# Performance work log

Hardware: AMD Instinct MI355X
Metric: run time of the kernel (lower is better)

## Reference

```python
import jax, jax.numpy as jnp
import numpy as np
from jax import lax

B_, H_, W_, C_ = 2, 64, 64, 96
DI, N_, R_, K_ = 192, 16, 6, 4  # d_inner=expand*C, d_state, dt_rank=ceil(96/16), 4 scan dirs


def _ln(x, g, b, eps):
    m = jnp.mean(x, axis=-1, keepdims=True)
    v = jnp.var(x, axis=-1, keepdims=True)
    return (x - m) / jnp.sqrt(v + eps) * g + b


def _conv1x1(x, w, b=None):
    y = jnp.einsum('bihw,oi->bohw', x, w)
    return y if b is None else y + b[None, :, None, None]


def _dwconv(x, w):
    return lax.conv_general_dilated(x, w, (1, 1), 'SAME',
                                    feature_group_count=x.shape[1],
                                    dimension_numbers=('NCHW', 'OIHW', 'NCHW'))


def _ss2d(x, in_proj_w, conv2d_w, conv2d_b, x_proj_w, dt_proj_w, dt_proj_b,
          A_logs, Ds, out_norm_g, out_norm_b, out_proj_w):
    B, H, W, C = x.shape
    L = H * W
    xz = jnp.einsum('bhwc,dc->bhwd', x, in_proj_w)          # [B,H,W,2*DI]
    xx, z = jnp.split(xz, 2, axis=-1)
    xc = jnp.transpose(xx, (0, 3, 1, 2))                    # [B,DI,H,W]
    xc = jax.nn.silu(_dwconv(xc, conv2d_w) + conv2d_b[None, :, None, None])
    # 4 scan directions: row-major, col-major, and their reverses
    x_hwwh = jnp.stack([xc.reshape(B, DI, L),
                        jnp.transpose(xc, (0, 1, 3, 2)).reshape(B, DI, L)], axis=1)
    xs = jnp.concatenate([x_hwwh, jnp.flip(x_hwwh, axis=-1)], axis=1)  # [B,K,DI,L]
    x_dbl = jnp.einsum('bkdl,kcd->bkcl', xs, x_proj_w)
    dts, Bs, Cs = jnp.split(x_dbl, [R_, R_ + N_], axis=2)   # [B,K,R,L],[B,K,N,L],[B,K,N,L]
    dt = jnp.einsum('bkrl,kdr->bkdl', dts, dt_proj_w) + dt_proj_b[None, :, :, None]
    dt = jax.nn.softplus(dt)
    A = -jnp.exp(A_logs).reshape(K_, DI, N_)

    def step(h, inp):
        u_t, dt_t, B_t, C_t = inp                            # [B,K,DI],[B,K,DI],[B,K,N],[B,K,N]
        dA = jnp.exp(dt_t[..., None] * A)                    # [B,K,DI,N]
        h = h * dA + (dt_t * u_t)[..., None] * B_t[:, :, None, :]
        y = jnp.einsum('bkdn,bkn->bkd', h, C_t)
        return h, y

    inps = (jnp.moveaxis(xs, -1, 0), jnp.moveaxis(dt, -1, 0),
            jnp.moveaxis(Bs, -1, 0), jnp.moveaxis(Cs, -1, 0))
    h0 = jnp.zeros((B, K_, DI, N_), xs.dtype)
    _, ys = lax.scan(step, h0, inps)                         # [L,B,K,DI]
    out_y = jnp.moveaxis(ys, 0, -1) + xs * Ds.reshape(K_, DI)[None, :, :, None]
    inv = jnp.flip(out_y[:, 2:4], axis=-1)
    y1 = out_y[:, 0]
    y2 = inv[:, 0]
    y3 = jnp.transpose(out_y[:, 1].reshape(B, DI, W, H), (0, 1, 3, 2)).reshape(B, DI, L)
    y4 = jnp.transpose(inv[:, 1].reshape(B, DI, W, H), (0, 1, 3, 2)).reshape(B, DI, L)
    y = jnp.transpose(y1 + y2 + y3 + y4, (0, 2, 1)).reshape(B, H, W, DI)
    y = _ln(y, out_norm_g, out_norm_b, 1e-5)
    y = y * jax.nn.silu(z)
    return jnp.einsum('bhwd,cd->bhwc', y, out_proj_w)


def _fftm(x, f1_w, f1_b, fm_w, fm_b, f2_w, f2_b):
    x = jax.nn.silu(_conv1x1(x, f1_w, f1_b))                 # [B,C/2,H,W]
    f = jnp.fft.rfftn(x, axes=(-2, -1), norm='ortho')        # [B,C/2,H,W//2+1] complex
    B, Ch, Hh, Wf = f.shape
    fr = jnp.stack([f.real, f.imag], axis=2).reshape(B, 2 * Ch, Hh, Wf)
    fr = jax.nn.silu(_conv1x1(fr, fm_w, fm_b))
    fr = fr.reshape(B, Ch, 2, Hh, Wf)
    fc = lax.complex(fr[:, :, 0], fr[:, :, 1])
    out = jnp.fft.irfftn(fc, s=x.shape[-2:], axes=(-2, -1), norm='ortho')
    return _conv1x1(out, f2_w, f2_b)


def _mgcb(x, in_w, dw3_w, dw5_w, out_w, ca_w1, ca_b1, ca_w2, ca_b2):
    Hd = 2 * x.shape[1]                                      # hidden_features = 2*dim
    p = _conv1x1(x, in_w)                                    # [B,2*Hd,H,W]
    s1 = 3 * Hd // 2
    x1, x2 = p[:, :s1], p[:, s1:]
    d1 = _dwconv(x1, dw3_w)
    x1_1, x1_2 = d1[:, :Hd], d1[:, Hd:]
    x2 = _dwconv(x2, dw5_w)
    y = jax.nn.gelu(x1_1, approximate=False) * jnp.concatenate([x1_2, x2], axis=1)
    y = _conv1x1(y, out_w)
    a = jnp.mean(y, axis=(2, 3))                             # channel attention (squeeze 30)
    a = jax.nn.relu(a @ ca_w1.T + ca_b1)
    a = jax.nn.sigmoid(a @ ca_w2.T + ca_b2)
    return y * a[:, :, None, None]


def _forward(input, ln1_g, ln1_b, skip_scale, skip_scale2, ln2_g, ln2_b,
             in_proj_w, conv2d_w, conv2d_b, x_proj_w, dt_proj_w, dt_proj_b,
             A_logs, Ds, out_norm_g, out_norm_b, out_proj_w,
             f1_w, f1_b, fm_w, fm_b, f2_w, f2_b,
             mg_in_w, mg_dw3_w, mg_dw5_w, mg_out_w,
             ca_w1, ca_b1, ca_w2, ca_b2, h_size, w_size):
    B, L, C = input.shape
    x4 = input.reshape(B, h_size, w_size, C)
    xn = _ln(x4, ln1_g, ln1_b, 1e-6)
    attn = _ss2d(xn, in_proj_w, conv2d_w, conv2d_b, x_proj_w, dt_proj_w,
                 dt_proj_b, A_logs, Ds, out_norm_g, out_norm_b, out_proj_w)
    fft = _fftm(jnp.transpose(xn, (0, 3, 1, 2)), f1_w, f1_b, fm_w, fm_b, f2_w, f2_b)
    x = x4 * skip_scale + attn + jnp.transpose(fft, (0, 2, 3, 1))
    xn2 = _ln(x, ln2_g, ln2_b, 1e-5)
    conv = _mgcb(jnp.transpose(xn2, (0, 3, 1, 2)), mg_in_w, mg_dw3_w, mg_dw5_w,
                 mg_out_w, ca_w1, ca_b1, ca_w2, ca_b2)
    x = x * skip_scale2 + jnp.transpose(conv, (0, 2, 3, 1))
    return x.reshape(B, L, C)


def setup_inputs() -> dict:
    key = jax.random.key(0)
    ks = iter(jax.random.split(key, 48))
    def rn(shape, s=0.02):
        return jax.random.normal(next(ks), shape, jnp.float32) * s
    d = {}
    d['input'] = jax.random.normal(next(ks), (B_, H_ * W_, C_), jnp.float32)
    d['ln1_g'] = jnp.ones((C_,)); d['ln1_b'] = jnp.zeros((C_,))
    d['skip_scale'] = jnp.ones((C_,)); d['skip_scale2'] = jnp.ones((C_,))
    d['ln2_g'] = jnp.ones((C_,)); d['ln2_b'] = jnp.zeros((C_,))
    d['in_proj_w'] = rn((2 * DI, C_))
    d['conv2d_w'] = rn((DI, 1, 3, 3), 0.1); d['conv2d_b'] = jnp.zeros((DI,))
    d['x_proj_w'] = rn((K_, R_ + 2 * N_, DI))
    d['dt_proj_w'] = rn((K_, DI, R_), 0.1)
    d['dt_proj_b'] = jnp.full((K_, DI), -4.6, jnp.float32) + rn((K_, DI), 0.5)
    d['A_logs'] = jnp.log(jnp.tile(jnp.arange(1, N_ + 1, dtype=jnp.float32), (K_ * DI, 1)))
    d['Ds'] = jnp.ones((K_ * DI,))
    d['out_norm_g'] = jnp.ones((DI,)); d['out_norm_b'] = jnp.zeros((DI,))
    d['out_proj_w'] = rn((C_, DI))
    Ch = C_ // 2
    d['f1_w'] = rn((Ch, C_)); d['f1_b'] = jnp.zeros((Ch,))
    d['fm_w'] = rn((C_, C_)); d['fm_b'] = jnp.zeros((C_,))
    d['f2_w'] = rn((C_, Ch)); d['f2_b'] = jnp.zeros((C_,))
    Hd = 2 * C_
    d['mg_in_w'] = rn((2 * Hd, C_))
    d['mg_dw3_w'] = rn((3 * Hd // 2, 1, 3, 3), 0.1)
    d['mg_dw5_w'] = rn((Hd // 2, 1, 5, 5), 0.1)
    d['mg_out_w'] = rn((C_, Hd))
    Csq = C_ // 30
    d['ca_w1'] = rn((Csq, C_)); d['ca_b1'] = jnp.zeros((Csq,))
    d['ca_w2'] = rn((C_, Csq)); d['ca_b2'] = jnp.zeros((C_,))
    d['h_size'] = H_
    d['w_size'] = W_
    return d


def reference(input, ln1_g, ln1_b, skip_scale, skip_scale2, ln2_g, ln2_b,
              in_proj_w, conv2d_w, conv2d_b, x_proj_w, dt_proj_w, dt_proj_b,
              A_logs, Ds, out_norm_g, out_norm_b, out_proj_w,
              f1_w, f1_b, fm_w, fm_b, f2_w, f2_b,
              mg_in_w, mg_dw3_w, mg_dw5_w, mg_out_w,
              ca_w1, ca_b1, ca_w2, ca_b2, h_size, w_size):
    return _forward(input, ln1_g, ln1_b, skip_scale, skip_scale2, ln2_g, ln2_b,
                    in_proj_w, conv2d_w, conv2d_b, x_proj_w, dt_proj_w, dt_proj_b,
                    A_logs, Ds, out_norm_g, out_norm_b, out_proj_w,
                    f1_w, f1_b, fm_w, fm_b, f2_w, f2_b,
                    mg_in_w, mg_dw3_w, mg_dw5_w, mg_out_w,
                    ca_w1, ca_b1, ca_w2, ca_b2, h_size, w_size)
```

## Files before the change

kernel.cpp:

```cpp
#include <hip/hip_runtime.h>
#include <math.h>

#define DEV __device__ __forceinline__

constexpr int DI = 192, Nn = 16, Rr = 6;
constexpr int Cc = 96;
constexpr int Ll = 4096;
constexpr int NC = 64;

DEV float silu_(float x) { return x / (1.f + __expf(-x)); }
DEV float wsum64(float v) {
  #pragma unroll
  for (int m = 32; m; m >>= 1) v += __shfl_xor(v, m, 64);
  return v;
}
DEV float qadd1(float v) {
  int i = __builtin_amdgcn_mov_dpp(__float_as_int(v), 0xB1, 0xF, 0xF, true);
  return v + __int_as_float(i);
}
DEV float qadd2(float v) {
  int i = __builtin_amdgcn_mov_dpp(__float_as_int(v), 0x4E, 0xF, 0xF, true);
  return v + __int_as_float(i);
}

template<int CIN, int COUT, int CB, int PXB, int IN_MODE, int OUT_MODE, int ACT, int HAS_BIAS, int LN>
__global__ void conv1x1v2_kernel(const float* __restrict__ in, const float4* __restrict__ wt,
                                 const float* __restrict__ bias, float* __restrict__ out,
                                 float* __restrict__ out2, const float* __restrict__ lng,
                                 const float* __restrict__ lnb) {
  constexpr int J4 = CIN / 4, STR = J4 + 1, CCN = CB / 16, PXT = PXB / 16;
  constexpr int NPB = 8192 / PXB;
  __shared__ float4 xv[PXB * STR];
  int t = threadIdx.x;
  int pb = blockIdx.x % NPB;
  int cbase = (blockIdx.x / NPB) * CB;
  int pbase = pb * PXB;
  if (IN_MODE == 0) {
    for (int idx = t; idx < PXB * J4; idx += 256) {
      int px = idx / J4, j4 = idx - px * J4;
      xv[px * STR + j4] = ((const float4*)in)[(size_t)(pbase + px) * J4 + j4];
    }
  } else {
    for (int idx = t; idx < PXB * CIN; idx += 256) {
      int px = idx & (PXB - 1), c = idx / PXB;
      int gp = pbase + px; int b = gp >> 12, p = gp & 4095;
      ((float*)xv)[px * (STR * 4) + c] = in[((size_t)b * CIN + c) * Ll + p];
    }
  }
  __syncthreads();
  if constexpr (LN) {
    constexpr int TPX = 256 / PXB;
    constexpr int CHUNK = CIN / TPX;
    int px = t / TPX, sub = t % TPX;
    float* row = (float*)(xv + px * STR);
    float sm = 0.f, sq = 0.f;
    #pragma unroll
    for (int j2 = 0; j2 < CHUNK; ++j2) {
      float v = row[sub + j2 * TPX];
      sm += v; sq += v * v;
    }
    #pragma unroll
    for (int m = 1; m < TPX; m <<= 1) {
      sm += __shfl_xor(sm, m, 64);
      sq += __shfl_xor(sq, m, 64);
    }
    float mean = sm * (1.f / CIN);
    float rs = rsqrtf(sq * (1.f / CIN) - mean * mean + 1e-6f);
    #pragma unroll
    for (int j2 = 0; j2 < CHUNK; ++j2) {
      int j = sub + j2 * TPX;
      row[j] = (row[j] - mean) * rs * lng[j] + lnb[j];
    }
    __syncthreads();
  }
  int g = t >> 4, ci = t & 15;
  float acc[PXT][CCN];
  #pragma unroll
  for (int cc = 0; cc < CCN; ++cc) {
    float b0 = HAS_BIAS ? bias[cbase + ci + 16 * cc] : 0.f;
    #pragma unroll
    for (int p = 0; p < PXT; ++p) acc[p][cc] = b0;
  }
  #pragma unroll 2
  for (int j4 = 0; j4 < J4; ++j4) {
    float4 xr[PXT];
    #pragma unroll
    for (int p = 0; p < PXT; ++p) xr[p] = xv[(g + 16 * p) * STR + j4];
    #pragma unroll
    for (int cc = 0; cc < CCN; ++cc) {
      float4 w4 = wt[(size_t)j4 * COUT + cbase + ci + 16 * cc];
      #pragma unroll
      for (int p = 0; p < PXT; ++p)
        acc[p][cc] += xr[p].x * w4.x + xr[p].y * w4.y + xr[p].z * w4.z + xr[p].w * w4.w;
    }
  }
  #pragma unroll
  for (int p = 0; p < PXT; ++p) {
    int gp = pbase + g + 16 * p;
    #pragma unroll
    for (int cc = 0; cc < CCN; ++cc) {
      int c = cbase + ci + 16 * cc;
      float v = acc[p][cc];
      if (OUT_MODE == 2) {
        if (c < 192) out[(size_t)gp * 192 + c] = v;
        else out2[(size_t)gp * 192 + (c - 192)] = silu_(v);
      } else {
        if (ACT == 1) v = silu_(v);
        if (OUT_MODE == 0) out[(size_t)gp * COUT + c] = v;
        else { int bb = gp >> 12, p2 = gp & 4095; out[((size_t)bb * COUT + c) * Ll + p2] = v; }
      }
    }
  }
}

__global__ void outproj_fused_kernel(
    const float* __restrict__ outy, const float* __restrict__ zs,
    const float* __restrict__ ong, const float* __restrict__ onb,
    const float4* __restrict__ wt, const float* __restrict__ input,
    const float* __restrict__ fftout, const float* __restrict__ ss,
    const float* __restrict__ ln2g, const float* __restrict__ ln2b,
    float* __restrict__ xres, float* __restrict__ xn2) {
  __shared__ float4 xv[32 * 49];
  int t = threadIdx.x;
  int pbase = blockIdx.x * 32;
  {
    int px = t >> 3, sub = t & 7;
    int pix = pbase + px;
    int p = pix & 4095, b = pix >> 12;
    int pt = ((p & 63) << 6) | (p >> 6);
    size_t base = (size_t)b * 4 * Ll * DI;
    const float* y0 = outy + base + (size_t)p * DI;
    const float* y1 = outy + base + ((size_t)Ll + pt) * DI;
    const float* y2 = outy + base + ((size_t)2 * Ll + (4095 - p)) * DI;
    const float* y3 = outy + base + ((size_t)3 * Ll + (4095 - pt)) * DI;
    float v[24];
    float sm = 0.f, sq = 0.f;
    #pragma unroll
    for (int j = 0; j < 24; ++j) {
      int c = sub + 8 * j;
      float vv = y0[c] + y1[c] + y2[c] + y3[c];
      v[j] = vv; sm += vv; sq += vv * vv;
    }
    #pragma unroll
    for (int m = 1; m < 8; m <<= 1) {
      sm += __shfl_xor(sm, m, 64);
      sq += __shfl_xor(sq, m, 64);
    }
    float mean = sm * (1.f / 192.f);
    float rs = rsqrtf(sq * (1.f / 192.f) - mean * mean + 1e-5f);
    const float* zrow = zs + (size_t)pix * DI;
    float* row = (float*)(xv + px * 49);
    #pragma unroll
    for (int j = 0; j < 24; ++j) {
      int c = sub + 8 * j;
      row[c] = ((v[j] - mean) * rs * ong[c] + onb[c]) * zrow[c];
    }
  }
  __syncthreads();
  int g = t >> 4, ci = t & 15;
  float acc[2][6];
  #pragma unroll
  for (int pI = 0; pI < 2; ++pI)
    #pragma unroll
    for (int cc = 0; cc < 6; ++cc) acc[pI][cc] = 0.f;
  #pragma unroll 2
  for (int j4 = 0; j4 < 48; ++j4) {
    float4 xr0 = xv[g * 49 + j4];
    float4 xr1 = xv[(g + 16) * 49 + j4];
    #pragma unroll
    for (int cc = 0; cc < 6; ++cc) {
      float4 w4 = wt[(size_t)j4 * 96 + ci + 16 * cc];
      acc[0][cc] += xr0.x * w4.x + xr0.y * w4.y + xr0.z * w4.z + xr0.w * w4.w;
      acc[1][cc] += xr1.x * w4.x + xr1.y * w4.y + xr1.z * w4.z + xr1.w * w4.w;
    }
  }
  #pragma unroll
  for (int pI = 0; pI < 2; ++pI) {
    int gp = pbase + g + 16 * pI;
    float vv[6];
    float sm = 0.f, sq = 0.f;
    #pragma unroll
    for (int cc = 0; cc < 6; ++cc) {
      int c = ci + 16 * cc;
      float x = input[(size_t)gp * Cc + c] * ss[c] + acc[pI][cc] + fftout[(size_t)gp * Cc + c];
      vv[cc] = x; sm += x; sq += x * x;
    }
    #pragma unroll
    for (int m = 1; m < 16; m <<= 1) {
      sm += __shfl_xor(sm, m, 64);
      sq += __shfl_xor(sq, m, 64);
    }
    float mean = sm * (1.f / 96.f);
    float rs = rsqrtf(sq * (1.f / 96.f) - mean * mean + 1e-5f);
    #pragma unroll
    for (int cc = 0; cc < 6; ++cc) {
      int c = ci + 16 * cc;
      xres[(size_t)gp * Cc + c] = vv[cc];
      xn2[(size_t)gp * Cc + c] = (vv[cc] - mean) * rs * ln2g[c] + ln2b[c];
    }
  }
}

__global__ void wprep_all_kernel(const float* __restrict__ xpw, float4* __restrict__ xpwT,
                                 const float* __restrict__ cw, const float* __restrict__ mg3,
                                 const float* __restrict__ mg5, float* __restrict__ WC3T,
                                 float* __restrict__ W3T, float* __restrict__ W5T,
                                 const float* __restrict__ ipw, float4* __restrict__ WIPT,
                                 const float* __restrict__ mgiw, float4* __restrict__ WMGT,
                                 const float* __restrict__ opw, float4* __restrict__ WOPT,
                                 const float* __restrict__ mgow, float4* __restrict__ WMOT,
                                 const float* __restrict__ f1w, float4* __restrict__ WF1T,
                                 const float* __restrict__ f2w, float4* __restrict__ WF2T) {
  int idx = blockIdx.x * 256 + threadIdx.x;
  if (idx < 9216) {
    int k = idx / (48 * 48);
    int r = idx % (48 * 48);
    int j4 = r / 48, c = r % 48;
    float4 v = make_float4(0.f, 0.f, 0.f, 0.f);
    if (c < 38) v = ((const float4*)xpw)[((size_t)k * 38 + c) * 48 + j4];
    xpwT[((size_t)k * 48 + j4) * 48 + c] = v;
  }
  if (idx < 1728) { int c = idx / 9, j = idx % 9; WC3T[j * 192 + c] = cw[idx]; }
  if (idx < 2592) { int c = idx / 9, j = idx % 9; W3T[j * 288 + c] = mg3[idx]; }
  if (idx < 2400) { int c = idx / 25, j = idx % 25; W5T[j * 96 + c] = mg5[idx]; }
  if (idx < 9216) { int oc = idx % 384, j4 = idx / 384; WIPT[idx] = ((const float4*)ipw)[(size_t)oc * 24 + j4]; }
  if (idx < 9216) { int oc = idx % 384, j4 = idx / 384; WMGT[idx] = ((const float4*)mgiw)[(size_t)oc * 24 + j4]; }
  if (idx < 4608) { int oc = idx % 96, j4 = idx / 96; WOPT[idx] = ((const float4*)opw)[(size_t)oc * 48 + j4]; }
  if (idx < 4608) { int oc = idx % 96, j4 = idx / 96; WMOT[idx] = ((const float4*)mgow)[(size_t)oc * 48 + j4]; }
  if (idx < 1152) { int oc = idx % 48, j4 = idx / 48; WF1T[idx] = ((const float4*)f1w)[(size_t)oc * 24 + j4]; }
  if (idx < 1152) { int oc = idx % 96, j4 = idx / 96; WF2T[idx] = ((const float4*)f2w)[(size_t)oc * 12 + j4]; }
}

__global__ void dwconv3_silu_kernel(const float* __restrict__ xx, const float* __restrict__ wc3t,
                                    const float* __restrict__ bias, float* __restrict__ xc,
                                    float* __restrict__ xct) {
  int idx = blockIdx.x * 256 + threadIdx.x;
  int d4 = idx % 48;
  int p = (idx / 48) & (Ll - 1);
  int b = idx / (48 * Ll);
  int h = p >> 6, wq = p & 63;
  const float4* base = (const float4*)xx + (size_t)b * Ll * 48;
  const float4* wt = (const float4*)wc3t;
  float4 bv = ((const float4*)bias)[d4];
  float a0 = bv.x, a1 = bv.y, a2 = bv.z, a3 = bv.w;
  #pragma unroll
  for (int i = 0; i < 3; ++i) {
    int hh = h - 1 + i;
    if ((unsigned)hh >= 64u) continue;
    #pragma unroll
    for (int j = 0; j < 3; ++j) {
      int ww2 = wq - 1 + j;
      if ((unsigned)ww2 >= 64u) continue;
      float4 x = base[(size_t)(hh * 64 + ww2) * 48 + d4];
      float4 w4 = wt[(i * 3 + j) * 48 + d4];
      a0 += x.x * w4.x; a1 += x.y * w4.y; a2 += x.z * w4.z; a3 += x.w * w4.w;
    }
  }
  float4 v = make_float4(silu_(a0), silu_(a1), silu_(a2), silu_(a3));
  ((float4*)xc)[idx] = v;
  int pt = (wq << 6) | h;
  ((float4*)xct)[((size_t)b * Ll + pt) * 48 + d4] = v;
}

__global__ void proj_kernel(const float* __restrict__ xc, const float4* __restrict__ xpwT,
                            float* __restrict__ BSo, float* __restrict__ CSo,
                            float* __restrict__ DTS) {
  __shared__ float4 xv[32 * 49];
  int t = threadIdx.x;
  int pb = blockIdx.x & 127;
  int k = (blockIdx.x >> 7) & 3;
  int b = blockIdx.x >> 9;
  int bk = b * 4 + k;
  int pbase = pb * 32;
  for (int idx = t; idx < 32 * 48; idx += 256) {
    int it = idx / 48, j4 = idx - it * 48;
    xv[it * 49 + j4] = ((const float4*)xc)[((size_t)b * Ll + pbase + it) * 48 + j4];
  }
  __syncthreads();
  int g = t >> 4, ci = t & 15;
  float acc[2][3];
  #pragma unroll
  for (int p = 0; p < 2; ++p)
    #pragma unroll
    for (int cc = 0; cc < 3; ++cc) acc[p][cc] = 0.f;
  #pragma unroll 2
  for (int j4 = 0; j4 < 48; ++j4) {
    float4 xr0 = xv[g * 49 + j4];
    float4 xr1 = xv[(g + 16) * 49 + j4];
    const float4* wrow = xpwT + ((size_t)k * 48 + j4) * 48;
    #pragma unroll
    for (int cc = 0; cc < 3; ++cc) {
      float4 w4 = wrow[ci + 16 * cc];
      acc[0][cc] += xr0.x * w4.x + xr0.y * w4.y + xr0.z * w4.z + xr0.w * w4.w;
      acc[1][cc] += xr1.x * w4.x + xr1.y * w4.y + xr1.z * w4.z + xr1.w * w4.w;
    }
  }
  #pragma unroll
  for (int pI = 0; pI < 2; ++pI) {
    int p = pbase + g + 16 * pI;
    int pt = ((p & 63) << 6) | (p >> 6);
    int l = (k == 0) ? p : (k == 1) ? pt : (k == 2) ? (4095 - p) : (4095 - pt);
    #pragma unroll
    for (int cc = 0; cc < 3; ++cc) {
      int c = ci + 16 * cc;
      float v = acc[pI][cc];
      if (c < 6) DTS[((size_t)bk * 6 + c) * Ll + l] = v;
      else if (c < 22) BSo[((size_t)bk * Ll + l) * Nn + (c - 6)] = v;
      else if (c < 38) CSo[((size_t)bk * Ll + l) * Nn + (c - 22)] = v;
    }
  }
}

__global__ void dtproj_kernel(const float* __restrict__ dts, const float* __restrict__ dtw,
                              const float* __restrict__ dtb, float* __restrict__ DTo) {
  __shared__ float sdts[6][64];
  int t = threadIdx.x;
  int lb = (blockIdx.x & 63) * 64;
  int bk = blockIdx.x >> 6;
  int k = bk & 3;
  if (t < 384) {
    int r = t / 64, l = t & 63;
    sdts[r][l] = dts[((size_t)bk * 6 + r) * Ll + lb + l];
  }
  __syncthreads();
  int d = t;
  const float* wr = dtw + ((size_t)k * DI + d) * Rr;
  float w0 = wr[0], w1 = wr[1], w2 = wr[2], w3 = wr[3], w4 = wr[4], w5 = wr[5];
  float b0 = dtb[k * DI + d];
  float* ob = DTo + ((size_t)bk * Ll + lb) * DI + d;
  #pragma unroll 4
  for (int l = 0; l < 64; ++l) {
    float a = b0 + sdts[0][l] * w0 + sdts[1][l] * w1 + sdts[2][l] * w2
            + sdts[3][l] * w3 + sdts[4][l] * w4 + sdts[5][l] * w5;
    float sp = (a > 20.f) ? a : log1pf(__expf(a));
    ob[(size_t)l * DI] = sp;
  }
}

__global__ void scanA_kernel(const float* __restrict__ dtg, const float* __restrict__ xc,
                             const float* __restrict__ xct, const float* __restrict__ bsg,
                             const float* __restrict__ alog,
                             float* __restrict__ P, float* __restrict__ Q) {
  int g = blockIdx.x * 256 + threadIdx.x;
  int ng = g & 3;
  int t1 = g >> 2;
  int d = t1 % DI;
  int t2 = t1 / DI;
  int c = t2 & 63;
  int bk = t2 >> 6;
  int k = bk & 3, b = bk >> 2;
  float4 al = ((const float4*)alog)[(size_t)(k * DI + d) * 4 + ng];
  float An0 = -__expf(al.x), An1 = -__expf(al.y), An2 = -__expf(al.z), An3 = -__expf(al.w);
  const float* dtp = dtg + ((size_t)bk * Ll + c * 64) * DI + d;
  const float4* bsp = (const float4*)bsg + ((size_t)bk * Ll + c * 64) * 4 + ng;
  const float* usrc = (k & 1) ? xct : xc;
  int p0 = (k >= 2) ? (4095 - c * 64) : (c * 64);
  int ustep = (k >= 2) ? -DI : DI;
  const float* up = usrc + ((size_t)b * Ll + p0) * DI + d;
  float P0 = 1.f, P1 = 1.f, P2 = 1.f, P3 = 1.f;
  float Q0 = 0.f, Q1 = 0.f, Q2 = 0.f, Q3 = 0.f;
  float dpre[4], upre[4];
  float4 bpre[4];
  #pragma unroll
  for (int i = 0; i < 4; ++i) {
    dpre[i] = dtp[(size_t)i * DI];
    upre[i] = up[(ptrdiff_t)i * ustep];
    bpre[i] = bsp[(size_t)i * 4];
  }
  for (int tg = 0; tg < 64; tg += 4) {
    #pragma unroll
    for (int i = 0; i < 4; ++i) {
      float dtv = dpre[i], u = upre[i];
      float4 Bv = bpre[i];
      int tn = tg + 4 + i;
      dpre[i] = dtp[(size_t)tn * DI];
      upre[i] = up[(ptrdiff_t)tn * ustep];
      bpre[i] = bsp[(size_t)tn * 4];
      float s = dtv * u;
      float a0 = __expf(dtv * An0), a1 = __expf(dtv * An1);
      float a2 = __expf(dtv * An2), a3 = __expf(dtv * An3);
      P0 *= a0; P1 *= a1; P2 *= a2; P3 *= a3;
      Q0 = Q0 * a0 + s * Bv.x; Q1 = Q1 * a1 + s * Bv.y;
      Q2 = Q2 * a2 + s * Bv.z; Q3 = Q3 * a3 + s * Bv.w;
    }
  }
  ((float4*)P)[g] = make_float4(P0, P1, P2, P3);
  ((float4*)Q)[g] = make_float4(Q0, Q1, Q2, Q3);
}

__global__ void scanB_kernel(const float* __restrict__ P, const float* __restrict__ Q,
                             float* __restrict__ H0) {
  int g = blockIdx.x * 256 + threadIdx.x;
  int n = g & 15;
  int d = (g >> 4) % DI;
  int bk = (g >> 4) / DI;
  size_t base = (size_t)bk * NC * DI * Nn + (size_t)d * Nn + n;
  float Ppre[4], Qpre[4];
  #pragma unroll
  for (int i = 0; i < 4; ++i) {
    Ppre[i] = P[base + (size_t)i * 3072];
    Qpre[i] = Q[base + (size_t)i * 3072];
  }
  float h = 0.f;
  for (int cg = 0; cg < 64; cg += 4) {
    #pragma unroll
    for (int i = 0; i < 4; ++i) {
      float pv = Ppre[i], qv = Qpre[i];
      Ppre[i] = P[base + (size_t)(cg + 4 + i) * 3072];
      Qpre[i] = Q[base + (size_t)(cg + 4 + i) * 3072];
      H0[base + (size_t)(cg + i) * 3072] = h;
      h = pv * h + qv;
    }
  }
}

__global__ void scanC_kernel(const float* __restrict__ dtg, const float* __restrict__ xc,
                             const float* __restrict__ xct, const float* __restrict__ bsg,
                             const float* __restrict__ csg, const float* __restrict__ alog,
                             const float* __restrict__ Dsv_, const float* __restrict__ H0,
                             float* __restrict__ outy) {
  int g = blockIdx.x * 256 + threadIdx.x;
  int ng = g & 3;
  int t1 = g >> 2;
  int d = t1 % DI;
  int t2 = t1 / DI;
  int c = t2 & 63;
  int bk = t2 >> 6;
  int k = bk & 3, b = bk >> 2;
  float4 al = ((const float4*)alog)[(size_t)(k * DI + d) * 4 + ng];
  float An0 = -__expf(al.x), An1 = -__expf(al.y), An2 = -__expf(al.z), An3 = -__expf(al.w);
  float Dsv = Dsv_[k * DI + d];
  const float* dtp = dtg + ((size_t)bk * Ll + c * 64) * DI + d;
  const float4* bsp = (const float4*)bsg + ((size_t)bk * Ll + c * 64) * 4 + ng;
  const float4* csp = (const float4*)csg + ((size_t)bk * Ll + c * 64) * 4 + ng;
  const float* usrc = (k & 1) ? xct : xc;
  int p0 = (k >= 2) ? (4095 - c * 64) : (c * 64);
  int ustep = (k >= 2) ? -DI : DI;
  const float* up = usrc + ((size_t)b * Ll + p0) * DI + d;
  float* yo = outy + ((size_t)bk * Ll + c * 64) * DI + d;
  float4 h4 = ((const float4*)H0)[g];
  float h0 = h4.x, h1 = h4.y, h2 = h4.z, h3 = h4.w;
  float dpre[4], upre[4];
  float4 bpre[4], cpre[4];
  #pragma unroll
  for (int i = 0; i < 4; ++i) {
    dpre[i] = dtp[(size_t)i * DI];
    upre[i] = up[(ptrdiff_t)i * ustep];
    bpre[i] = bsp[(size_t)i * 4];
    cpre[i] = csp[(size_t)i * 4];
  }
  for (int tg = 0; tg < 64; tg += 4) {
    #pragma unroll
    for (int i = 0; i < 4; ++i) {
      float dtv = dpre[i], u = upre[i];
      float4 Bv = bpre[i], Cv = cpre[i];
      int tn = tg + 4 + i;
      dpre[i] = dtp[(size_t)tn * DI];
      upre[i] = up[(ptrdiff_t)tn * ustep];
      bpre[i] = bsp[(size_t)tn * 4];
      cpre[i] = csp[(size_t)tn * 4];
      float s = dtv * u;
      float a0 = __expf(dtv * An0), a1 = __expf(dtv * An1);
      float a2 = __expf(dtv * An2), a3 = __expf(dtv * An3);
      h0 = h0 * a0 + s * Bv.x; h1 = h1 * a1 + s * Bv.y;
      h2 = h2 * a2 + s * Bv.z; h3 = h3 * a3 + s * Bv.w;
      float yp = h0 * Cv.x + h1 * Cv.y + h2 * Cv.z + h3 * Cv.w;
      yp = qadd1(yp);
      yp = qadd2(yp);
      if (ng == 0) yo[(size_t)(tg + i) * DI] = yp + u * Dsv;
    }
  }
}

__global__ void dft_row_kernel(const float* __restrict__ xf, float* __restrict__ Tr,
                               float* __restrict__ Ti) {
  __shared__ float row[4][64];
  __shared__ float cs[64], sn[64];
  int t = threadIdx.x, lane = t & 63, wv = t >> 6;
  int bch = blockIdx.x * 4 + wv;
  row[wv][lane] = xf[(size_t)bch * 64 + lane];
  if (t < 64) {
    float ang = (float)t * 0.09817477042468103f;
    float s0, c0; sincosf(ang, &s0, &c0); sn[t] = s0; cs[t] = c0;
  }
  __syncthreads();
  if (lane < 33) {
    float ar = 0.f, ai = 0.f;
    for (int wq = 0; wq < 64; ++wq) {
      int j = (lane * wq) & 63;
      ar += row[wv][wq] * cs[j];
      ai -= row[wv][wq] * sn[j];
    }
    Tr[(size_t)bch * 33 + lane] = ar;
    Ti[(size_t)bch * 33 + lane] = ai;
  }
}

__global__ void dft_col_kernel(const float* __restrict__ Tr, const float* __restrict__ Ti,
                               float* __restrict__ Gr, float* __restrict__ Gi) {
  __shared__ float tr[4][64], ti[4][64];
  __shared__ float cs[64], sn[64];
  int t = threadIdx.x, lane = t & 63, wv = t >> 6;
  int idx = blockIdx.x * 4 + wv;
  int v = idx % 33, bc = idx / 33;
  tr[wv][lane] = Tr[((size_t)bc * 64 + lane) * 33 + v];
  ti[wv][lane] = Ti[((size_t)bc * 64 + lane) * 33 + v];
  if (t < 64) {
    float ang = (float)t * 0.09817477042468103f;
    float s0, c0; sincosf(ang, &s0, &c0); sn[t] = s0; cs[t] = c0;
  }
  __syncthreads();
  float ar = 0.f, ai = 0.f;
  for (int hh = 0; hh < 64; ++hh) {
    int j = (lane * hh) & 63;
    ar += tr[wv][hh] * cs[j] + ti[wv][hh] * sn[j];
    ai += ti[wv][hh] * cs[j] - tr[wv][hh] * sn[j];
  }
  Gr[((size_t)bc * 64 + lane) * 33 + v] = ar * (1.f / 64.f);
  Gi[((size_t)bc * 64 + lane) * 33 + v] = ai * (1.f / 64.f);
}

__global__ void fmix2_kernel(const float* __restrict__ Gr, const float* __restrict__ Gi,
                             const float* __restrict__ w, const float* __restrict__ bias,
                             float* __restrict__ Mr, float* __restrict__ Mi) {
  __shared__ float xs[16][100];
  int t = threadIdx.x;
  int uvb = (blockIdx.x % 132) * 16;
  int b = blockIdx.x / 132;
  for (int idx = t; idx < 96 * 16; idx += 256) {
    int ch = idx >> 4, px = idx & 15;
    const float* src = (ch & 1) ? Gi : Gr;
    xs[px][ch] = src[((size_t)(b * 48 + (ch >> 1))) * 2112 + uvb + px];
  }
  __syncthreads();
  int px = t >> 4, ci = t & 15;
  float acc[6];
  #pragma unroll
  for (int cc = 0; cc < 6; ++cc) acc[cc] = bias[ci + 16 * cc];
  const float4* xr4 = (const float4*)&xs[px][0];
  #pragma unroll 2
  for (int j4 = 0; j4 < 24; ++j4) {
    float4 x4 = xr4[j4];
    #pragma unroll
    for (int cc = 0; cc < 6; ++cc) {
      float4 w4 = ((const float4*)w)[(size_t)(ci + 16 * cc) * 24 + j4];
      acc[cc] += x4.x * w4.x + x4.y * w4.y + x4.z * w4.z + x4.w * w4.w;
    }
  }
  int uv = uvb + px;
  #pragma unroll
  for (int cc = 0; cc < 6; ++cc) {
    int o = ci + 16 * cc;
    float v = silu_(acc[cc]);
    float* dst = (o & 1) ? Mi : Mr;
    dst[((size_t)(b * 48 + (o >> 1))) * 2112 + uv] = v;
  }
}

__global__ void idft_col_kernel(const float* __restrict__ Mr, const float* __restrict__ Mi,
                                float* __restrict__ gr, float* __restrict__ gi) {
  __shared__ float mr[4][64], mi[4][64];
  __shared__ float cs[64], sn[64];
  int t = threadIdx.x, lane = t & 63, wv = t >> 6;
  int idx = blockIdx.x * 4 + wv;
  int v = idx % 33, bc = idx / 33;
  mr[wv][lane] = Mr[((size_t)bc * 64 + lane) * 33 + v];
  mi[wv][lane] = Mi[((size_t)bc * 64 + lane) * 33 + v];
  if (t < 64) {
    float ang = (float)t * 0.09817477042468103f;
    float s0, c0; sincosf(ang, &s0, &c0); sn[t] = s0; cs[t] = c0;
  }
  __syncthreads();
  float ar = 0.f, ai = 0.f;
  for (int u = 0; u < 64; ++u) {
    int j = (lane * u) & 63;
    ar += mr[wv][u] * cs[j] - mi[wv][u] * sn[j];
    ai += mr[wv][u] * sn[j] + mi[wv][u] * cs[j];
  }
  gr[((size_t)bc * 64 + lane) * 33 + v] = ar;
  gi[((size_t)bc * 64 + lane) * 33 + v] = ai;
}

__global__ void irfft_row_kernel(const float* __restrict__ gr, const float* __restrict__ gi,
                                 float* __restrict__ ysp) {
  __shared__ float r[4][33], im[4][33];
  __shared__ float cs[64], sn[64];
  int t = threadIdx.x, lane = t & 63, wv = t >> 6;
  int bch = blockIdx.x * 4 + wv;
  if (lane < 33) {
    r[wv][lane] = gr[(size_t)bch * 33 + lane];
    im[wv][lane] = gi[(size_t)bch * 33 + lane];
  }
  if (t < 64) {
    float ang = (float)t * 0.09817477042468103f;
    float s0, c0; sincosf(ang, &s0, &c0); sn[t] = s0; cs[t] = c0;
  }
  __syncthreads();
  float acc = r[wv][0] + ((lane & 1) ? -r[wv][32] : r[wv][32]);
  for (int v = 1; v < 32; ++v) {
    int j = (v * lane) & 63;
    acc += 2.f * (r[wv][v] * cs[j] - im[wv][v] * sn[j]);
  }
  ysp[(size_t)bch * 64 + lane] = acc * (1.f / 64.f);
}

__global__ void mgcb_dw_kernel(const float* __restrict__ pm, const float* __restrict__ w3t,
                               const float* __restrict__ w5t, float* __restrict__ ymg) {
  int idx = blockIdx.x * 256 + threadIdx.x;
  int c4 = idx % 48;
  int p = (idx / 48) & (Ll - 1);
  int b = idx / (48 * Ll);
  int h = p >> 6, wq = p & 63;
  const float4* base = (const float4*)pm + (size_t)b * Ll * 96;
  const float4* wt3 = (const float4*)w3t;
  float g0 = 0.f, g1 = 0.f, g2 = 0.f, g3 = 0.f;
  float m0 = 0.f, m1 = 0.f, m2 = 0.f, m3 = 0.f;
  if (c4 < 24) {
    #pragma unroll
    for (int i = 0; i < 3; ++i) {
      int hh = h - 1 + i; if ((unsigned)hh >= 64u) continue;
      #pragma unroll
      for (int j = 0; j < 3; ++j) {
        int ww2 = wq - 1 + j; if ((unsigned)ww2 >= 64u) continue;
        const float4* px = base + (size_t)(hh * 64 + ww2) * 96;
        float4 xg = px[c4];
        float4 wg = wt3[(i * 3 + j) * 72 + c4];
        g0 += xg.x * wg.x; g1 += xg.y * wg.y; g2 += xg.z * wg.z; g3 += xg.w * wg.w;
        float4 xm = px[48 + c4];
        float4 wm = wt3[(i * 3 + j) * 72 + 48 + c4];
        m0 += xm.x * wm.x; m1 += xm.y * wm.y; m2 += xm.z * wm.z; m3 += xm.w * wm.w;
      }
    }
  } else {
    #pragma unroll
    for (int i = 0; i < 3; ++i) {
      int hh = h - 1 + i; if ((unsigned)hh >= 64u) continue;
      #pragma unroll
      for (int j = 0; j < 3; ++j) {
        int ww2 = wq - 1 + j; if ((unsigned)ww2 >= 64u) continue;
        float4 xg = base[(size_t)(hh * 64 + ww2) * 96 + c4];
        float4 wg = wt3[(i * 3 + j) * 72 + c4];
        g0 += xg.x * wg.x; g1 += xg.y * wg.y; g2 += xg.z * wg.z; g3 += xg.w * wg.w;
      }
    }
    const float4* wt5 = (const float4*)w5t;
    int cw4 = c4 - 24;
    #pragma unroll
    for (int i = 0; i < 5; ++i) {
      int hh = h - 2 + i; if ((unsigned)hh >= 64u) continue;
      #pragma unroll
      for (int j = 0; j < 5; ++j) {
        int ww2 = wq - 2 + j; if ((unsigned)ww2 >= 64u) continue;
        float4 xm = base[(size_t)(hh * 64 + ww2) * 96 + 48 + c4];
        float4 wm = wt5[(i * 5 + j) * 24 + cw4];
        m0 += xm.x * wm.x; m1 += xm.y * wm.y; m2 += xm.z * wm.z; m3 += xm.w * wm.w;
      }
    }
  }
  const float IS2 = 0.70710678118654752f;
  float4 o;
  o.x = 0.5f * g0 * (1.f + erff(g0 * IS2)) * m0;
  o.y = 0.5f * g1 * (1.f + erff(g1 * IS2)) * m1;
  o.z = 0.5f * g2 * (1.f + erff(g2 * IS2)) * m2;
  o.w = 0.5f * g3 * (1.f + erff(g3 * IS2)) * m3;
  ((float4*)ymg)[idx] = o;
}

__global__ void camean1_kernel(const float* __restrict__ yc, float* __restrict__ partial) {
  __shared__ float red[192];
  int t = threadIdx.x;
  int blk = blockIdx.x;
  int b = blk >> 4, ptile = blk & 15;
  int px = t / 96, c = t - 96 * px;
  const float* src = yc + ((size_t)b * Ll + ptile * 256) * Cc + c;
  float s = 0.f;
  for (int it = 0; it < 128; ++it)
    s += src[(size_t)(it * 2 + px) * Cc];
  red[t] = s;
  __syncthreads();
  if (t < 96) partial[((size_t)b * 16 + ptile) * 96 + t] = red[t] + red[t + 96];
}

__global__ void camean2_kernel(const float* __restrict__ partial, float* __restrict__ means) {
  int c = threadIdx.x;
  int b = blockIdx.x;
  float s = 0.f;
  #pragma unroll
  for (int i = 0; i < 16; ++i) s += partial[((size_t)b * 16 + i) * 96 + c];
  means[b * 96 + c] = s * (1.f / 4096.f);
}

__global__ void camlp_kernel(const float* __restrict__ means, const float* __restrict__ w1,
                             const float* __restrict__ b1, const float* __restrict__ w2,
                             const float* __restrict__ b2, float* __restrict__ avec) {
  int c = threadIdx.x;
  if (c >= 96) return;
  for (int b = 0; b < 2; ++b) {
    float t[3];
    #pragma unroll
    for (int j = 0; j < 3; ++j) {
      float a = b1[j];
      for (int cc = 0; cc < 96; ++cc) a += means[b * 96 + cc] * w1[j * 96 + cc];
      t[j] = fmaxf(a, 0.f);
    }
    float a2 = b2[c];
    #pragma unroll
    for (int j = 0; j < 3; ++j) a2 += t[j] * w2[c * 3 + j];
    avec[b * 96 + c] = 1.f / (1.f + expf(-a2));
  }
}

__global__ void final_kernel(const float* __restrict__ xres, const float* __restrict__ yc,
                             const float* __restrict__ ss2, const float* __restrict__ avec,
                             float* __restrict__ out) {
  int idx = blockIdx.x * 256 + threadIdx.x;
  int c = idx % 96;
  int b = idx / (Ll * 96);
  out[idx] = xres[idx] * ss2[c] + yc[idx] * avec[b * 96 + c];
}

extern "C" void kernel_launch(void* const* d_in, const int* in_sizes, int n_in,
                              void* d_out, int out_size, void* d_ws, size_t ws_size,
                              hipStream_t stream) {
  const float* input      = (const float*)d_in[0];
  const float* ln1_g      = (const float*)d_in[1];
  const float* ln1_b      = (const float*)d_in[2];
  const float* skip_scale = (const float*)d_in[3];
  const float* skip_scale2= (const float*)d_in[4];
  const float* ln2_g      = (const float*)d_in[5];
  const float* ln2_b      = (const float*)d_in[6];
  const float* in_proj_w  = (const float*)d_in[7];
  const float* conv2d_w   = (const float*)d_in[8];
  const float* conv2d_b   = (const float*)d_in[9];
  const float* x_proj_w   = (const float*)d_in[10];
  const float* dt_proj_w  = (const float*)d_in[11];
  const float* dt_proj_b  = (const float*)d_in[12];
  const float* A_logs     = (const float*)d_in[13];
  const float* Ds         = (const float*)d_in[14];
  const float* out_norm_g = (const float*)d_in[15];
  const float* out_norm_b = (const float*)d_in[16];
  const float* out_proj_w = (const float*)d_in[17];
  const float* f1_w       = (const float*)d_in[18];
  const float* f1_b       = (const float*)d_in[19];
  const float* fm_w       = (const float*)d_in[20];
  const float* fm_b       = (const float*)d_in[21];
  const float* f2_w       = (const float*)d_in[22];
  const float* f2_b       = (const float*)d_in[23];
  const float* mg_in_w    = (const float*)d_in[24];
  const float* mg_dw3_w   = (const float*)d_in[25];
  const float* mg_dw5_w   = (const float*)d_in[26];
  const float* mg_out_w   = (const float*)d_in[27];
  const float* ca_w1      = (const float*)d_in[28];
  const float* ca_b1      = (const float*)d_in[29];
  const float* ca_w2      = (const float*)d_in[30];
  const float* ca_b2      = (const float*)d_in[31];

  float* W = (float*)d_ws;
  float* XN    = W;
  float* ZSILU = XN + 786432;
  float* XX    = ZSILU + 1572864;
  float* XC    = XX + 1572864;
  float* XCT   = XC + 1572864;
  float* DT    = XCT + 1572864;
  float* BSb   = DT + 6291456;
  float* CSb   = BSb + 524288;
  float* PP    = CSb + 524288;
  float* QQ    = PP + 1572864;
  float* H0    = QQ + 1572864;
  float* OUTY  = H0 + 1572864;
  float* YGATE = OUTY + 6291456;
  float* ATTN  = YGATE + 1572864;
  float* FFTOUT= ATTN + 786432;
  float* XRES  = FFTOUT + 786432;
  float* XN2   = XRES + 786432;
  float* MEANS = XN2 + 786432;
  float* AVEC  = MEANS + 192;
  float* XPWT  = AVEC + 192;
  float* WC3T  = XPWT + 36864;
  float* W3T   = WC3T + 1728;
  float* W5T   = W3T + 2592;
  float* CAP   = W5T + 2400;
  float* WIPT  = CAP + 3072;
  float* WMGT  = WIPT + 36864;
  float* WOPT  = WMGT + 36864;
  float* WMOT  = WOPT + 18432;
  float* WF1T  = WMOT + 18432;
  float* WF2T  = WF1T + 4608;
  float* DTS = H0;
  float* XF  = PP;
  float* TR  = XF + 393216;
  float* TI  = TR + 202752;
  float* GR  = TI + 202752;
  float* GI  = GR + 202752;
  float* MR  = TR;
  float* MI  = TI;
  float* G2R = GR;
  float* G2I = GI;
  float* YSP = GI + 202752;
  float* PMG = DT;
  float* YMG = DT + 3145728;
  float* YCb = YMG + 1572864;

  wprep_all_kernel<<<36, 256, 0, stream>>>(
      x_proj_w, (float4*)XPWT, conv2d_w, mg_dw3_w, mg_dw5_w, WC3T, W3T, W5T,
      in_proj_w, (float4*)WIPT, mg_in_w, (float4*)WMGT, out_proj_w, (float4*)WOPT,
      mg_out_w, (float4*)WMOT, f1_w, (float4*)WF1T, f2_w, (float4*)WF2T);
  conv1x1v2_kernel<96, 384, 96, 64, 0, 2, 0, 0, 1><<<512, 256, 0, stream>>>(
      input, (const float4*)WIPT, nullptr, XX, ZSILU, ln1_g, ln1_b);
  dwconv3_silu_kernel<<<1536, 256, 0, stream>>>(XX, WC3T, conv2d_b, XC, XCT);
  proj_kernel<<<1024, 256, 0, stream>>>(XC, (const float4*)XPWT, BSb, CSb, DTS);
  dtproj_kernel<<<512, 192, 0, stream>>>(DTS, dt_proj_w, dt_proj_b, DT);
  scanA_kernel<<<1536, 256, 0, stream>>>(DT, XC, XCT, BSb, A_logs, PP, QQ);
  scanB_kernel<<<96, 256, 0, stream>>>(PP, QQ, H0);
  conv1x1v2_kernel<96, 48, 48, 32, 0, 1, 1, 1, 1><<<256, 256, 0, stream>>>(
      input, (const float4*)WF1T, f1_b, XF, nullptr, ln1_g, ln1_b);
  dft_row_kernel<<<1536, 256, 0, stream>>>(XF, TR, TI);
  dft_col_kernel<<<792, 256, 0, stream>>>(TR, TI, GR, GI);
  fmix2_kernel<<<264, 256, 0, stream>>>(GR, GI, fm_w, fm_b, MR, MI);
  idft_col_kernel<<<792, 256, 0, stream>>>(MR, MI, G2R, G2I);
  irfft_row_kernel<<<1536, 256, 0, stream>>>(G2R, G2I, YSP);
  conv1x1v2_kernel<48, 96, 96, 32, 1, 0, 0, 1, 0><<<256, 256, 0, stream>>>(
      YSP, (const float4*)WF2T, f2_b, FFTOUT, nullptr, nullptr, nullptr);
  scanC_kernel<<<1536, 256, 0, stream>>>(DT, XC, XCT, BSb, CSb, A_logs, Ds, H0, OUTY);
  outproj_fused_kernel<<<256, 256, 0, stream>>>(
      OUTY, ZSILU, out_norm_g, out_norm_b, (const float4*)WOPT, input, FFTOUT,
      skip_scale, ln2_g, ln2_b, XRES, XN2);
  conv1x1v2_kernel<96, 384, 96, 64, 0, 0, 0, 0, 0><<<512, 256, 0, stream>>>(
      XN2, (const float4*)WMGT, nullptr, PMG, nullptr, nullptr, nullptr);
  mgcb_dw_kernel<<<1536, 256, 0, stream>>>(PMG, W3T, W5T, YMG);
  conv1x1v2_kernel<192, 96, 96, 32, 0, 0, 0, 0, 0><<<256, 256, 0, stream>>>(
      YMG, (const float4*)WMOT, nullptr, YCb, nullptr, nullptr, nullptr);
  camean1_kernel<<<32, 192, 0, stream>>>(YCb, CAP);
  camean2_kernel<<<2, 96, 0, stream>>>(CAP, MEANS);
  camlp_kernel<<<1, 128, 0, stream>>>(MEANS, ca_w1, ca_b1, ca_w2, ca_b2, AVEC);
  final_kernel<<<3072, 256, 0, stream>>>(XRES, YCb, skip_scale2, AVEC, (float*)d_out);
}
```

Baseline: 370.6 us.

## Fuse channel-attention pooling into output conv and transpose DFT intermediates

Replaces the mg_out 1x1 conv plus three channel-attention kernels with a single conv kernel that also writes per-block channel partial sums, followed by one merge kernel that finishes the means and runs the small MLP. This removes a separate pass over the conv output and two launches. It also transposes the layout of the DFT intermediates (Tr/Ti, Mr/Mi) so the column DFT kernels read contiguous data instead of strided data. The cost moves to the row DFT and fmix kernels, whose writes become strided, and the merge kernel runs as a single block.

```diff
diff --git a/kernel.cpp b/kernel.cpp
--- a/kernel.cpp
+++ b/kernel.cpp
@@ -9,11 +9,6 @@
 constexpr int NC = 64;
 
 DEV float silu_(float x) { return x / (1.f + __expf(-x)); }
-DEV float wsum64(float v) {
-  #pragma unroll
-  for (int m = 32; m; m >>= 1) v += __shfl_xor(v, m, 64);
-  return v;
-}
 DEV float qadd1(float v) {
   int i = __builtin_amdgcn_mov_dpp(__float_as_int(v), 0xB1, 0xF, 0xF, true);
   return v + __int_as_float(i);
@@ -198,6 +193,90 @@
       xres[(size_t)gp * Cc + c] = vv[cc];
       xn2[(size_t)gp * Cc + c] = (vv[cc] - mean) * rs * ln2g[c] + ln2b[c];
     }
+  }
+}
+
+__global__ void mgout_fused_kernel(const float* __restrict__ in, const float4* __restrict__ wt,
+                                   float* __restrict__ out, float* __restrict__ cap) {
+  __shared__ float4 xv[32 * 49];
+  __shared__ float redc[4][96];
+  int t = threadIdx.x;
+  int pbase = blockIdx.x * 32;
+  for (int idx = t; idx < 32 * 48; idx += 256) {
+    int px = idx / 48, j4 = idx - px * 48;
+    xv[px * 49 + j4] = ((const float4*)in)[(size_t)(pbase + px) * 48 + j4];
+  }
+  __syncthreads();
+  int g = t >> 4, ci = t & 15;
+  float acc[2][6];
+  #pragma unroll
+  for (int pI = 0; pI < 2; ++pI)
+    #pragma unroll
+    for (int cc = 0; cc < 6; ++cc) acc[pI][cc] = 0.f;
+  #pragma unroll 2
+  for (int j4 = 0; j4 < 48; ++j4) {
+    float4 xr0 = xv[g * 49 + j4];
+    float4 xr1 = xv[(g + 16) * 49 + j4];
+    #pragma unroll
+    for (int cc = 0; cc < 6; ++cc) {
+      float4 w4 = wt[(size_t)j4 * 96 + ci + 16 * cc];
+      acc[0][cc] += xr0.x * w4.x + xr0.y * w4.y + xr0.z * w4.z + xr0.w * w4.w;
+      acc[1][cc] += xr1.x * w4.x + xr1.y * w4.y + xr1.z * w4.z + xr1.w * w4.w;
+    }
+  }
+  float ps[6];
+  #pragma unroll
+  for (int cc = 0; cc < 6; ++cc) ps[cc] = acc[0][cc] + acc[1][cc];
+  #pragma unroll
+  for (int pI = 0; pI < 2; ++pI) {
+    int gp = pbase + g + 16 * pI;
+    #pragma unroll
+    for (int cc = 0; cc < 6; ++cc)
+      out[(size_t)gp * 96 + ci + 16 * cc] = acc[pI][cc];
+  }
+  #pragma unroll
+  for (int cc = 0; cc < 6; ++cc) {
+    ps[cc] += __shfl_xor(ps[cc], 16, 64);
+    ps[cc] += __shfl_xor(ps[cc], 32, 64);
+  }
+  if ((t & 63) < 16) {
+    #pragma unroll
+    for (int cc = 0; cc < 6; ++cc) redc[t >> 6][ci + 16 * cc] = ps[cc];
+  }
+  __syncthreads();
+  if (t < 96)
+    cap[(size_t)blockIdx.x * 96 + t] = redc[0][t] + redc[1][t] + redc[2][t] + redc[3][t];
+}
+
+__global__ void camerge_kernel(const float* __restrict__ cap, const float* __restrict__ w1,
+                               const float* __restrict__ b1, const float* __restrict__ w2,
+                               const float* __restrict__ b2, float* __restrict__ avec) {
+  __shared__ float red[4][192];
+  __shared__ float means[192];
+  int t = threadIdx.x;
+  int q = t / 192, r = t % 192;
+  int b = r / 96, c = r % 96;
+  float s = 0.f;
+  for (int j = 0; j < 32; ++j)
+    s += cap[(size_t)(b * 128 + q * 32 + j) * 96 + c];
+  red[q][r] = s;
+  __syncthreads();
+  if (t < 192)
+    means[t] = (red[0][t] + red[1][t] + red[2][t] + red[3][t]) * (1.f / 4096.f);
+  __syncthreads();
+  if (t < 192) {
+    int bb = t / 96, cc2 = t % 96;
+    float tt[3];
+    #pragma unroll
+    for (int j = 0; j < 3; ++j) {
+      float a = b1[j];
+      for (int cc = 0; cc < 96; ++cc) a += means[bb * 96 + cc] * w1[j * 96 + cc];
+      tt[j] = fmaxf(a, 0.f);
+    }
+    float a2 = b2[cc2];
+    #pragma unroll
+    for (int j = 0; j < 3; ++j) a2 += tt[j] * w2[cc2 * 3 + j];
+    avec[t] = 1.f / (1.f + expf(-a2));
   }
 }
 
@@ -478,6 +557,7 @@
   __shared__ float cs[64], sn[64];
   int t = threadIdx.x, lane = t & 63, wv = t >> 6;
   int bch = blockIdx.x * 4 + wv;
+  int h = bch & 63, bc = bch >> 6;
   row[wv][lane] = xf[(size_t)bch * 64 + lane];
   if (t < 64) {
     float ang = (float)t * 0.09817477042468103f;
@@ -491,8 +571,8 @@
       ar += row[wv][wq] * cs[j];
       ai -= row[wv][wq] * sn[j];
     }
-    Tr[(size_t)bch * 33 + lane] = ar;
-    Ti[(size_t)bch * 33 + lane] = ai;
+    Tr[((size_t)bc * 33 + lane) * 64 + h] = ar;
+    Ti[((size_t)bc * 33 + lane) * 64 + h] = ai;
   }
 }
 
@@ -503,8 +583,8 @@
   int t = threadIdx.x, lane = t & 63, wv = t >> 6;
   int idx = blockIdx.x * 4 + wv;
   int v = idx % 33, bc = idx / 33;
-  tr[wv][lane] = Tr[((size_t)bc * 64 + lane) * 33 + v];
-  ti[wv][lane] = Ti[((size_t)bc * 64 + lane) * 33 + v];
+  tr[wv][lane] = Tr[((size_t)bc * 33 + v) * 64 + lane];
+  ti[wv][lane] = Ti[((size_t)bc * 33 + v) * 64 + lane];
   if (t < 64) {
     float ang = (float)t * 0.09817477042468103f;
     float s0, c0; sincosf(ang, &s0, &c0); sn[t] = s0; cs[t] = c0;
@@ -548,12 +628,13 @@
     }
   }
   int uv = uvb + px;
+  int u = uv / 33, vv2 = uv % 33;
   #pragma unroll
   for (int cc = 0; cc < 6; ++cc) {
     int o = ci + 16 * cc;
     float v = silu_(acc[cc]);
     float* dst = (o & 1) ? Mi : Mr;
-    dst[((size_t)(b * 48 + (o >> 1))) * 2112 + uv] = v;
+    dst[((size_t)(b * 48 + (o >> 1))) * 2112 + vv2 * 64 + u] = v;
   }
 }
 
@@ -564,8 +645,8 @@
   int t = threadIdx.x, lane = t & 63, wv = t >> 6;
   int idx = blockIdx.x * 4 + wv;
   int v = idx % 33, bc = idx / 33;
-  mr[wv][lane] = Mr[((size_t)bc * 64 + lane) * 33 + v];
-  mi[wv][lane] = Mi[((size_t)bc * 64 + lane) * 33 + v];
+  mr[wv][lane] = Mr[((size_t)bc * 33 + v) * 64 + lane];
+  mi[wv][lane] = Mi[((size_t)bc * 33 + v) * 64 + lane];
   if (t < 64) {
     float ang = (float)t * 0.09817477042468103f;
     float s0, c0; sincosf(ang, &s0, &c0); sn[t] = s0; cs[t] = c0;
@@ -664,50 +745,6 @@
   o.z = 0.5f * g2 * (1.f + erff(g2 * IS2)) * m2;
   o.w = 0.5f * g3 * (1.f + erff(g3 * IS2)) * m3;
   ((float4*)ymg)[idx] = o;
-}
-
-__global__ void camean1_kernel(const float* __restrict__ yc, float* __restrict__ partial) {
-  __shared__ float red[192];
-  int t = threadIdx.x;
-  int blk = blockIdx.x;
-  int b = blk >> 4, ptile = blk & 15;
-  int px = t / 96, c = t - 96 * px;
-  const float* src = yc + ((size_t)b * Ll + ptile * 256) * Cc + c;
-  float s = 0.f;
-  for (int it = 0; it < 128; ++it)
-    s += src[(size_t)(it * 2 + px) * Cc];
-  red[t] = s;
-  __syncthreads();
-  if (t < 96) partial[((size_t)b * 16 + ptile) * 96 + t] = red[t] + red[t + 96];
-}
-
-__global__ void camean2_kernel(const float* __restrict__ partial, float* __restrict__ means) {
-  int c = threadIdx.x;
-  int b = blockIdx.x;
-  float s = 0.f;
-  #pragma unroll
-  for (int i = 0; i < 16; ++i) s += partial[((size_t)b * 16 + i) * 96 + c];
-  means[b * 96 + c] = s * (1.f / 4096.f);
-}
-
-__global__ void camlp_kernel(const float* __restrict__ means, const float* __restrict__ w1,
-                             const float* __restrict__ b1, const float* __restrict__ w2,
-                             const float* __restrict__ b2, float* __restrict__ avec) {
-  int c = threadIdx.x;
-  if (c >= 96) return;
-  for (int b = 0; b < 2; ++b) {
-    float t[3];
-    #pragma unroll
-    for (int j = 0; j < 3; ++j) {
-      float a = b1[j];
-      for (int cc = 0; cc < 96; ++cc) a += means[b * 96 + cc] * w1[j * 96 + cc];
-      t[j] = fmaxf(a, 0.f);
-    }
-    float a2 = b2[c];
-    #pragma unroll
-    for (int j = 0; j < 3; ++j) a2 += t[j] * w2[c * 3 + j];
-    avec[b * 96 + c] = 1.f / (1.f + expf(-a2));
-  }
 }
 
 __global__ void final_kernel(const float* __restrict__ xres, const float* __restrict__ yc,
@@ -780,7 +817,7 @@
   float* W3T   = WC3T + 1728;
   float* W5T   = W3T + 2592;
   float* CAP   = W5T + 2400;
-  float* WIPT  = CAP + 3072;
+  float* WIPT  = CAP + 24576;
   float* WMGT  = WIPT + 36864;
   float* WOPT  = WMGT + 36864;
   float* WMOT  = WOPT + 18432;
@@ -828,10 +865,7 @@
   conv1x1v2_kernel<96, 384, 96, 64, 0, 0, 0, 0, 0><<<512, 256, 0, stream>>>(
       XN2, (const float4*)WMGT, nullptr, PMG, nullptr, nullptr, nullptr);
   mgcb_dw_kernel<<<1536, 256, 0, stream>>>(PMG, W3T, W5T, YMG);
-  conv1x1v2_kernel<192, 96, 96, 32, 0, 0, 0, 0, 0><<<256, 256, 0, stream>>>(
-      YMG, (const float4*)WMOT, nullptr, YCb, nullptr, nullptr, nullptr);
-  camean1_kernel<<<32, 192, 0, stream>>>(YCb, CAP);
-  camean2_kernel<<<2, 96, 0, stream>>>(CAP, MEANS);
-  camlp_kernel<<<1, 128, 0, stream>>>(MEANS, ca_w1, ca_b1, ca_w2, ca_b2, AVEC);
+  mgout_fused_kernel<<<256, 256, 0, stream>>>(YMG, (const float4*)WMOT, YCb, CAP);
+  camerge_kernel<<<1, 768, 0, stream>>>(CAP, ca_w1, ca_b1, ca_w2, ca_b2, AVEC);
   final_kernel<<<3072, 256, 0, stream>>>(XRES, YCb, skip_scale2, AVEC, (float*)d_out);
 }
```

New measurement: 346.4 us. -6.5%, faster.
